# Kernel tuning notes

Measured on AMD Instinct MI355X. Metric: run time of the kernel, lower is better.

The kernel has to match this reference:

```python
import jax, jax.numpy as jnp
import numpy as np

N_CLASSES = 16
B, N = 8, 2048
F = [128, 512, 1024]
K = [6, 5, 3]
M = [512, 128, 50]
IN_DIM = 22


def get_laplacian(x):
    # exp(-squared pairwise distance) adjacency, then normalized Laplacian I - D^-1/2 A D^-1/2
    inner = jnp.matmul(x, x.transpose(0, 2, 1))            # [B,N,N]
    sq = jnp.sum(x * x, axis=-1, keepdims=True)            # [B,N,1]
    adj = jnp.exp(-(sq - 2.0 * inner + sq.transpose(0, 2, 1)))
    dinv = 1.0 / jnp.sqrt(jnp.sum(adj, axis=-1))           # [B,N]
    Lnorm = dinv[:, :, None] * adj * dinv[:, None, :]
    return jnp.eye(x.shape[1], dtype=x.dtype) - Lnorm


def cheb_conv(x, L, W, b):
    # Chebyshev recursion: x0=x, x1=Lx, x_k = 2 L x_{k-1} - x_{k-2}; out = sum_k x_k @ W_k + b
    Kk = W.shape[0]
    x0 = x
    out = jnp.einsum('bni,io->bno', x0, W[0])
    if Kk > 1:
        x1 = jnp.matmul(L, x0)
        out = out + jnp.einsum('bni,io->bno', x1, W[1])
        for k in range(2, Kk):
            x2 = 2.0 * jnp.matmul(L, x1) - x0
            out = out + jnp.einsum('bni,io->bno', x2, W[k])
            x0, x1 = x1, x2
    return out + b


def setup_inputs() -> dict:
    key = jax.random.key(0)
    ks = jax.random.split(key, 24)
    d = {}
    d['x'] = jax.random.normal(ks[0], (B, N, 6), dtype=jnp.float32)
    d['cat'] = jax.random.randint(ks[1], (B, 1), 0, N_CLASSES)
    ins = [IN_DIM, F[0], F[1]]
    for i in range(3):
        s = 1.0 / np.sqrt(ins[i] * K[i])
        d[f'cheb_w{i}'] = jax.random.normal(ks[2 + i], (K[i], ins[i], F[i]), dtype=jnp.float32) * s
        d[f'cheb_b{i}'] = jnp.zeros((F[i],), dtype=jnp.float32)
    fc_ins = [F[-1], M[0] + M[0], M[1]]
    for i in range(3):
        s = 1.0 / np.sqrt(fc_ins[i])
        d[f'fc_w{i}'] = jax.random.normal(ks[6 + i], (fc_ins[i], M[i]), dtype=jnp.float32) * s
        d[f'fc_b{i}'] = jax.random.normal(ks[10 + i], (M[i],), dtype=jnp.float32) * s
    relus = F + M
    for i in range(6):
        d[f'br{i}'] = jnp.zeros((1, N, relus[i]), dtype=jnp.float32)
    return d


def reference(x, cat, cheb_w0, cheb_b0, cheb_w1, cheb_b1, cheb_w2, cheb_b2,
              fc_w0, fc_b0, fc_w1, fc_b1, fc_w2, fc_b2,
              br0, br1, br2, br3, br4, br5):
    L = jax.lax.stop_gradient(get_laplacian(x))  # torch.no_grad in original
    cat_oh = jax.nn.one_hot(cat, N_CLASSES, dtype=x.dtype)      # [B,1,16]
    cat_oh = jnp.tile(cat_oh, (1, N, 1))                         # [B,N,16]
    out = jnp.concatenate([x, cat_oh], axis=2)                   # [B,N,22]

    cheb_ws = [cheb_w0, cheb_w1, cheb_w2]
    cheb_bs = [cheb_b0, cheb_b1, cheb_b2]
    brs = [br0, br1, br2, br3, br4, br5]
    x1 = None
    for i in range(3):
        out = cheb_conv(out, L, cheb_ws[i], cheb_bs[i])
        out = jax.nn.relu(out + brs[i])  # dropout is identity in eval
        if i == 1:
            x1 = out

    fc_ws = [fc_w0, fc_w1, fc_w2]
    fc_bs = [fc_b0, fc_b1, fc_b2]
    for i in range(3):
        if i == 1:
            out = jnp.concatenate([out, x1], axis=2)
        out = jnp.einsum('bni,io->bno', out, fc_ws[i]) + fc_bs[i]
        out = jax.nn.relu(out + brs[i + 3])
    return out
```

## Files before the change

### kernel.cpp

```cpp
#include <hip/hip_runtime.h>
#include <stdint.h>

typedef __attribute__((ext_vector_type(8))) short short8;
typedef __attribute__((ext_vector_type(4))) float f32x4;

#define DEV __device__ __forceinline__

DEV ushort f2bf(float f){ uint32_t u = __float_as_uint(f); u += 0x7fffu + ((u >> 16) & 1u); return (ushort)(u >> 16); }
DEV float bf2f(ushort h){ return __uint_as_float(((uint32_t)h) << 16); }

template<int N> DEV void wvm(){
    asm volatile("s_waitcnt vmcnt(%0)" :: "i"(N) : "memory");
}


__global__ void wt_kernel(const float* __restrict__ src, ushort* __restrict__ dst,
                          int I, int O, int Opad, int blk, int srcF){
    int idx = blockIdx.x * 256 + threadIdx.x;
    if (idx >= Opad * I) return;
    int i = idx % I, o = idx / I;
    int k = i / blk, f = i % blk;
    ushort v = 0;
    if (o < O && f < srcF) v = f2bf(src[((long)k * srcF + f) * O + o]);
    dst[idx] = v;
}

__global__ void x0t_kernel(const float* __restrict__ x, const int* __restrict__ cat,
                           ushort* __restrict__ dst){
    int idx = blockIdx.x * 256 + threadIdx.x;
    int n = idx & 2047, f = (idx >> 11) & 31, b = idx >> 16;
    ushort v = 0;
    if (f < 6) v = f2bf(x[((long)b * 2048 + n) * 6 + f]);
    else if (f < 22) v = (cat[b] == f - 6) ? (ushort)0x3f80 : (ushort)0;
    dst[idx] = v;
}

__global__ void xt_kernel(const float* __restrict__ x, float* __restrict__ xT){
    int idx = blockIdx.x * 256 + threadIdx.x;
    if (idx >= 16384) return;
    int b = idx >> 11, n = idx & 2047;
    float* dst = xT + (long)b * 6 * 2048 + n;
#pragma unroll
    for (int d = 0; d < 6; d++) dst[d * 2048] = x[(long)idx * 6 + d];
}

__global__ __launch_bounds__(256) void dinv_kernel(const float* __restrict__ xT, float* __restrict__ dinv){
    int b = blockIdx.y;
    int wave = threadIdx.x >> 6, lane = threadIdx.x & 63;
    int i0 = blockIdx.x * 16 + wave * 4;
    const float* xtb = xT + (long)b * 6 * 2048;
    float xi[4][6];
#pragma unroll
    for (int ii = 0; ii < 4; ii++)
#pragma unroll
        for (int d = 0; d < 6; d++) xi[ii][d] = xtb[d * 2048 + i0 + ii];
    float s[4] = {0.f, 0.f, 0.f, 0.f};
#pragma unroll 2
    for (int jj = 0; jj < 32; jj++){
        int j = jj * 64 + lane;
        float xd[6];
#pragma unroll
        for (int d = 0; d < 6; d++) xd[d] = xtb[d * 2048 + j];
#pragma unroll
        for (int ii = 0; ii < 4; ii++){
            float a = 0.0f;
#pragma unroll
            for (int d = 0; d < 6; d++){ float t = xi[ii][d] - xd[d]; a += t * t; }
            s[ii] += __expf(-a);
        }
    }
#pragma unroll
    for (int ii = 0; ii < 4; ii++){
#pragma unroll
        for (int o = 32; o > 0; o >>= 1) s[ii] += __shfl_xor(s[ii], o);
    }
    if (lane == 0){
#pragma unroll
        for (int ii = 0; ii < 4; ii++) dinv[(b << 11) + i0 + ii] = rsqrtf(s[ii]);
    }
}

__global__ __launch_bounds__(256) void lap_kernel(const float* __restrict__ x, const float* __restrict__ dinv,
                                                  ushort* __restrict__ L){
    int b = blockIdx.z;
    int i0 = blockIdx.y * 32 + (threadIdx.x >> 6) * 8;
    int j0 = blockIdx.x * 512 + (threadIdx.x & 63) * 8;
    const float* xb = x + (long)b * 2048 * 6;
    const float* dv = dinv + (b << 11);
    f32x4 v[12];
    const f32x4* src = (const f32x4*)(xb + (long)j0 * 6);
#pragma unroll
    for (int c = 0; c < 12; c++) v[c] = src[c];
    const float* xj = (const float*)v;
    f32x4 dj0 = *(const f32x4*)(dv + j0);
    f32x4 dj1 = *(const f32x4*)(dv + j0 + 4);
    float dj[8] = {dj0[0], dj0[1], dj0[2], dj0[3], dj1[0], dj1[1], dj1[2], dj1[3]};
    ushort* out = L + ((long)b << 22) + (long)i0 * 2048 + j0;
#pragma unroll
    for (int ii = 0; ii < 8; ii++){
        const int i = i0 + ii;
        float xi[6];
#pragma unroll
        for (int d = 0; d < 6; d++) xi[d] = xb[i * 6 + d];
        const float di = dv[i];
        short8 o;
#pragma unroll
        for (int jj = 0; jj < 8; jj++){
            float a = 0.0f;
#pragma unroll
            for (int d = 0; d < 6; d++){ float t = xi[d] - xj[jj * 6 + d]; a += t * t; }
            float val = -di * dj[jj] * __expf(-a);
            if (i == j0 + jj) val += 1.0f;
            o[jj] = (short)f2bf(val);
        }
        *(short8*)(out + (long)ii * 2048) = o;
    }
}

__global__ void ts_kernel(const ushort* __restrict__ src, ushort* __restrict__ dst,
                          int F, int KF){
    int b = blockIdx.z;
    int i0 = blockIdx.y * 32;
    int k = i0 / F, f0 = i0 % F;
    int n0 = blockIdx.x * 64;
    __shared__ ushort t[32][66];
    const ushort* s = src + (((long)k * 8 + b) * F + f0) * 2048 + n0;
    int r = threadIdx.x >> 3, c8 = (threadIdx.x & 7) * 8;
    *(short8*)&t[r][c8] = *(const short8*)(s + (long)r * 2048 + c8);
    __syncthreads();
    int c = threadIdx.x >> 2, r8 = (threadIdx.x & 3) * 8;
    short8 v;
#pragma unroll
    for (int j = 0; j < 8; j++) v[j] = (short)t[r8 + j][c];
    *(short8*)(dst + ((long)b * 2048 + n0 + c) * KF + i0 + r8) = v;
}

__global__ void copy_x1_kernel(const ushort* __restrict__ src, ushort* __restrict__ dst){
    int idx = blockIdx.x * 256 + threadIdx.x;
    int r = idx >> 6, c = (idx & 63) * 8;
    *(short8*)(dst + (long)r * 1024 + 512 + c) = *(const short8*)(src + (long)r * 1536 + c);
}

template<int BM, int BN, int WR, int WC, int MODE>
__global__ __launch_bounds__(256) void gemm2(
    const ushort* __restrict__ A, int lda, long sA,
    const ushort* __restrict__ BT, int ldb, long sB,
    ushort* __restrict__ C, int ldc, long sC,
    int K,
    const ushort* __restrict__ Xp, long sX,
    const float* __restrict__ bias, const float* __restrict__ br, int brF,
    float* __restrict__ outF)
{
    constexpr int WM = BM / WR, WN = BN / WC, FM = WM / 16, FN = WN / 16;
    constexpr int ACH = BM / 16;
    constexpr int NCH = (BM + BN) / 16;
    __shared__ __align__(16) ushort As[BM * 32];
    __shared__ __align__(16) ushort Bs[BN * 32];
    const int tid = threadIdx.x, lane = tid & 63, wave = tid >> 6;
    const int wr = wave / WC, wc = wave % WC;
    const int bm0 = blockIdx.x * BM, bn0 = blockIdx.y * BN;
    const long z = blockIdx.z;
    A += z * sA; BT += z * sB;
    if (MODE != 4) C += z * sC;
    if (MODE == 1) Xp += z * sX;

    f32x4 acc[FM][FN];
#pragma unroll
    for (int m = 0; m < FM; m++)
#pragma unroll
        for (int n = 0; n < FN; n++) acc[m][n] = f32x4{0.f, 0.f, 0.f, 0.f};

    const int crow = lane >> 2;
    const int ccol = (lane & 3) * 8;

    for (int kt = 0; kt < K; kt += 32){
#pragma unroll
        for (int c = wave; c < NCH; c += 4){
            const ushort* gsrc;
            ushort* ldst;
            if (c < ACH){
                ldst = &As[c * 512];
                gsrc = A + (long)(bm0 + c * 16 + crow) * lda + kt + ccol;
            } else {
                ldst = &Bs[(c - ACH) * 512];
                gsrc = BT + (long)(bn0 + (c - ACH) * 16 + crow) * ldb + kt + ccol;
            }
            __builtin_amdgcn_global_load_lds(
                (const __attribute__((address_space(1))) void*)gsrc,
                (__attribute__((address_space(3))) void*)ldst, 16, 0, 0);
        }
        __syncthreads();
        const int kg = (lane >> 4) * 8;
        short8 af[FM], bfr[FN];
#pragma unroll
        for (int m = 0; m < FM; m++)
            af[m] = *(const short8*)&As[(wr * WM + m * 16 + (lane & 15)) * 32 + kg];
#pragma unroll
        for (int n = 0; n < FN; n++)
            bfr[n] = *(const short8*)&Bs[(wc * WN + n * 16 + (lane & 15)) * 32 + kg];
#pragma unroll
        for (int m = 0; m < FM; m++)
#pragma unroll
            for (int n = 0; n < FN; n++)
                acc[m][n] = __builtin_amdgcn_mfma_f32_16x16x32_bf16(af[m], bfr[n], acc[m][n], 0, 0, 0);
        __syncthreads();
    }

#pragma unroll
    for (int m = 0; m < FM; m++){
        const int r0 = bm0 + wr * WM + m * 16 + ((lane >> 4) << 2);
#pragma unroll
        for (int n = 0; n < FN; n++){
            const int col = bn0 + wc * WN + n * 16 + (lane & 15);
#pragma unroll
            for (int j = 0; j < 4; j++){
                const int r = r0 + j;
                float v = acc[m][n][j];
                if (MODE == 0){
                    C[(long)r * ldc + col] = f2bf(v);
                } else if (MODE == 1){
                    float p = bf2f(Xp[(long)r * ldc + col]);
                    C[(long)r * ldc + col] = f2bf(2.0f * v - p);
                } else if (MODE == 2){
                    float o = v + bias[r] + br[(long)col * brF + r];
                    C[(long)r * ldc + col] = f2bf(fmaxf(o, 0.0f));
                } else if (MODE == 3){
                    float o = v + bias[col] + br[(long)(r & 2047) * brF + col];
                    C[(long)r * ldc + col] = f2bf(fmaxf(o, 0.0f));
                } else {
                    if (col < 50){
                        float o = v + bias[col] + br[(long)(r & 2047) * 50 + col];
                        outF[(long)r * 50 + col] = fmaxf(o, 0.0f);
                    }
                }
            }
        }
    }
}

template<int BM, int BN, int MODE>
__global__ __launch_bounds__(256) void gmv(
    const ushort* __restrict__ A, int lda, long sA,
    const ushort* __restrict__ BT, int ldb, long sB,
    ushort* __restrict__ C, int ldc, long sC,
    int K,
    const ushort* __restrict__ Xp, long sX)
{
    constexpr int WM = BM / 2, WN = BN / 2, FM = WM / 16, FN = WN / 16;
    constexpr int ACH = BM / 8;
    constexpr int NCH = (BM + BN) / 8;
    constexpr int LPW = NCH / 4;
    static_assert(NCH % 4 == 0, "uniform loads per wave");
    __shared__ __align__(16) ushort lds[3 * (BM + BN) * 64];
    const int tid = threadIdx.x, lane = tid & 63, wave = tid >> 6;
    const int wr = wave >> 1, wc = wave & 1;
    const long z = blockIdx.x;
    const int bm0 = blockIdx.y * BM, bn0 = blockIdx.z * BN;
    A += z * sA; BT += z * sB; C += z * sC;
    if (MODE == 1) Xp += z * sX;
    const int NT = K >> 6;

    const int srow = lane >> 3;
    const int kloc = ((lane & 7) ^ srow) * 8;

    auto stage = [&](int u, int sel){
        ushort* dst0 = lds + sel * (BM + BN) * 64;
#pragma unroll
        for (int i = 0; i < LPW; i++){
            int c = i * 4 + wave;
            ushort* ldst = dst0 + c * 512;
            const ushort* src;
            if (c < ACH) src = A + (long)(bm0 + c * 8 + srow) * lda + u * 64 + kloc;
            else         src = BT + (long)(bn0 + (c - ACH) * 8 + srow) * ldb + u * 64 + kloc;
            __builtin_amdgcn_global_load_lds(
                (const __attribute__((address_space(1))) void*)src,
                (__attribute__((address_space(3))) void*)ldst, 16, 0, 0);
        }
    };

    f32x4 acc[FM][FN];
#pragma unroll
    for (int m = 0; m < FM; m++)
#pragma unroll
        for (int n = 0; n < FN; n++) acc[m][n] = f32x4{0.f, 0.f, 0.f, 0.f};

    stage(0, 0);
    if (NT > 1) stage(1, 1);

    int sel = 0;
    for (int u = 0; u < NT; u++){
        if (u + 1 < NT) wvm<LPW>(); else wvm<0>();
        __builtin_amdgcn_sched_barrier(0);
        __builtin_amdgcn_s_barrier();
        __builtin_amdgcn_sched_barrier(0);
        const char* base = (const char*)lds + sel * (BM + BN) * 128;
        const int hi = (lane >> 4) << 4;
        short8 af[FM], bfr[FN];
#pragma unroll
        for (int h = 0; h < 2; h++){
            const int kb = h * 64 + hi;
#pragma unroll
            for (int m = 0; m < FM; m++){
                int row = wr * WM + m * 16 + (lane & 15);
                af[m] = *(const short8*)(base + row * 128 + (kb ^ ((row & 7) << 4)));
            }
#pragma unroll
            for (int n = 0; n < FN; n++){
                int row = BM + wc * WN + n * 16 + (lane & 15);
                bfr[n] = *(const short8*)(base + row * 128 + (kb ^ ((row & 7) << 4)));
            }
            __builtin_amdgcn_s_setprio(1);
#pragma unroll
            for (int m = 0; m < FM; m++)
#pragma unroll
                for (int n = 0; n < FN; n++)
                    acc[m][n] = __builtin_amdgcn_mfma_f32_16x16x32_bf16(af[m], bfr[n], acc[m][n], 0, 0, 0);
            __builtin_amdgcn_s_setprio(0);
        }
        if (u + 2 < NT) stage(u + 2, (u + 2) % 3);
        sel = (sel == 2) ? 0 : sel + 1;
    }

#pragma unroll
    for (int m = 0; m < FM; m++){
        const int r0 = bm0 + wr * WM + m * 16 + ((lane >> 4) << 2);
#pragma unroll
        for (int n = 0; n < FN; n++){
            const int col = bn0 + wc * WN + n * 16 + (lane & 15);
#pragma unroll
            for (int j = 0; j < 4; j++){
                const int r = r0 + j;
                float v = acc[m][n][j];
                if (MODE == 0){
                    C[(long)r * ldc + col] = f2bf(v);
                } else {
                    float p = bf2f(Xp[(long)r * ldc + col]);
                    C[(long)r * ldc + col] = f2bf(2.0f * v - p);
                }
            }
        }
    }
}

template<int MODE, int SWZ>
__global__ __launch_bounds__(256) void gd(
    const ushort* __restrict__ A, int lda, long sA,
    const ushort* __restrict__ BT, int ldb, long sB,
    ushort* __restrict__ C, int ldc, long sC,
    int K,
    const ushort* __restrict__ Xp, long sX,
    const float* __restrict__ bias, const float* __restrict__ br, int brF)
{
    __shared__ __align__(16) ushort lds[2 * 256 * 64];
    const int tid = threadIdx.x, lane = tid & 63, wave = tid >> 6;
    const int wr = wave >> 1, wc = wave & 1;
    const int bm0 = (SWZ ? blockIdx.y : blockIdx.x) * 128;
    const int bn0 = (SWZ ? blockIdx.z : blockIdx.y) * 128;
    const long z = SWZ ? blockIdx.x : blockIdx.z;
    A += z * sA; BT += z * sB; C += z * sC;
    if (MODE == 1) Xp += z * sX;
    const int NT = K >> 6;

    const int srow = lane >> 3;
    const int kloc = ((lane & 7) ^ srow) * 8;

    auto stage = [&](int u, int sel){
        ushort* dst0 = lds + sel * 16384;
#pragma unroll
        for (int i = 0; i < 8; i++){
            int c = i * 4 + wave;
            const ushort* src = (c < 16)
                ? A + (long)(bm0 + c * 8 + srow) * lda + (long)u * 64 + kloc
                : BT + (long)(bn0 + (c - 16) * 8 + srow) * ldb + (long)u * 64 + kloc;
            __builtin_amdgcn_global_load_lds(
                (const __attribute__((address_space(1))) void*)src,
                (__attribute__((address_space(3))) void*)(dst0 + c * 512), 16, 0, 0);
        }
    };

    f32x4 acc[4][4];
#pragma unroll
    for (int m = 0; m < 4; m++)
#pragma unroll
        for (int n = 0; n < 4; n++) acc[m][n] = f32x4{0.f, 0.f, 0.f, 0.f};

    stage(0, 0);
    if (NT > 1) stage(1, 1);
    wvm<8>();
    __builtin_amdgcn_sched_barrier(0);
    __builtin_amdgcn_s_barrier();
    __builtin_amdgcn_sched_barrier(0);

    for (int u = 0; u < NT; u++){
        const char* Ab = (const char*)lds + (u & 1) * 32768;
        const char* Bb = Ab + 16384;
        const int hi = (lane >> 4) << 4;
        short8 af[4], bf[4];
#pragma unroll
        for (int m = 0; m < 4; m++){
            int row = wr * 64 + m * 16 + (lane & 15);
            af[m] = *(const short8*)(Ab + row * 128 + (hi ^ ((row & 7) << 4)));
        }
#pragma unroll
        for (int n = 0; n < 4; n++){
            int row = wc * 64 + n * 16 + (lane & 15);
            bf[n] = *(const short8*)(Bb + row * 128 + (hi ^ ((row & 7) << 4)));
        }
        if (u >= 1 && u + 1 < NT) stage(u + 1, (u + 1) & 1);
        __builtin_amdgcn_s_setprio(1);
#pragma unroll
        for (int m = 0; m < 4; m++)
#pragma unroll
            for (int n = 0; n < 4; n++)
                acc[m][n] = __builtin_amdgcn_mfma_f32_16x16x32_bf16(af[m], bf[n], acc[m][n], 0, 0, 0);
        __builtin_amdgcn_s_setprio(0);
#pragma unroll
        for (int m = 0; m < 4; m++){
            int row = wr * 64 + m * 16 + (lane & 15);
            af[m] = *(const short8*)(Ab + row * 128 + ((64 + hi) ^ ((row & 7) << 4)));
        }
#pragma unroll
        for (int n = 0; n < 4; n++){
            int row = wc * 64 + n * 16 + (lane & 15);
            bf[n] = *(const short8*)(Bb + row * 128 + ((64 + hi) ^ ((row & 7) << 4)));
        }
        __builtin_amdgcn_s_setprio(1);
#pragma unroll
        for (int m = 0; m < 4; m++)
#pragma unroll
            for (int n = 0; n < 4; n++)
                acc[m][n] = __builtin_amdgcn_mfma_f32_16x16x32_bf16(af[m], bf[n], acc[m][n], 0, 0, 0);
        __builtin_amdgcn_s_setprio(0);
        wvm<0>();
        __builtin_amdgcn_sched_barrier(0);
        __builtin_amdgcn_s_barrier();
        __builtin_amdgcn_sched_barrier(0);
    }

#pragma unroll
    for (int m = 0; m < 4; m++){
        const int r0 = bm0 + wr * 64 + m * 16 + ((lane >> 4) << 2);
#pragma unroll
        for (int n = 0; n < 4; n++){
            const int col = bn0 + wc * 64 + n * 16 + (lane & 15);
#pragma unroll
            for (int j = 0; j < 4; j++){
                const int r = r0 + j;
                float v = acc[m][n][j];
                if (MODE == 0){
                    C[(long)r * ldc + col] = f2bf(v);
                } else if (MODE == 1){
                    float p = bf2f(Xp[(long)r * ldc + col]);
                    C[(long)r * ldc + col] = f2bf(2.0f * v - p);
                } else if (MODE == 2){
                    float o = v + bias[r] + br[(long)col * brF + r];
                    C[(long)r * ldc + col] = f2bf(fmaxf(o, 0.0f));
                } else {
                    float o = v + bias[col] + br[(long)(r & 2047) * brF + col];
                    C[(long)r * ldc + col] = f2bf(fmaxf(o, 0.0f));
                }
            }
        }
    }
}


extern "C" void kernel_launch(void* const* d_in, const int* in_sizes, int n_in,
                              void* d_out, int out_size, void* d_ws, size_t ws_size,
                              hipStream_t stream){
    const float* x   = (const float*)d_in[0];
    const int*   cat = (const int*)d_in[1];
    const float* cw0 = (const float*)d_in[2];
    const float* cb0 = (const float*)d_in[3];
    const float* cw1 = (const float*)d_in[4];
    const float* cb1 = (const float*)d_in[5];
    const float* cw2 = (const float*)d_in[6];
    const float* cb2 = (const float*)d_in[7];
    const float* fw0 = (const float*)d_in[8];
    const float* fb0 = (const float*)d_in[9];
    const float* fw1 = (const float*)d_in[10];
    const float* fb1 = (const float*)d_in[11];
    const float* fw2 = (const float*)d_in[12];
    const float* fb2 = (const float*)d_in[13];
    const float* br0 = (const float*)d_in[14];
    const float* br1 = (const float*)d_in[15];
    const float* br2 = (const float*)d_in[16];
    const float* br3 = (const float*)d_in[17];
    const float* br4 = (const float*)d_in[18];
    const float* br5 = (const float*)d_in[19];
    float* out = (float*)d_out;
    (void)in_sizes; (void)n_in; (void)out_size; (void)ws_size;

    char* ws = (char*)d_ws;
    long off = 0;
    auto take = [&](long bytes){ char* p = ws + off; off += (bytes + 255) & ~255L; return p; };
    ushort* Lb   = (ushort*)take(8L * 2048 * 2048 * 2);
    float*  din  = (float*) take(8L * 2048 * 4);
    float*  XT   = (float*) take(8L * 6 * 2048 * 4);
    ushort* W0T  = (ushort*)take(128L * 192 * 2);
    ushort* W1T  = (ushort*)take(512L * 640 * 2);
    ushort* W2T  = (ushort*)take(1024L * 1536 * 2);
    ushort* WF0T = (ushort*)take(512L * 1024 * 2);
    ushort* WF1T = (ushort*)take(128L * 1024 * 2);
    ushort* WF2T = (ushort*)take(64L * 128 * 2);
    ushort* ST0T = (ushort*)take(6L * 8 * 32 * 2048 * 2);
    ushort* S0   = (ushort*)take(16384L * 192 * 2);
    ushort* ST1T = (ushort*)take(5L * 8 * 128 * 2048 * 2);
    ushort* S1   = (ushort*)take(16384L * 640 * 2);
    ushort* ST2T = (ushort*)take(3L * 8 * 512 * 2048 * 2);
    ushort* S2   = (ushort*)take(16384L * 1536 * 2);
    ushort* X3 = Lb;
    ushort* CC = ST2T;
    ushort* H5 = ST0T;

    const long NN = 2048L * 2048;
    const long s0k = 8L * 32 * 2048,  s0b = 32L * 2048;
    const long s1k = 8L * 128 * 2048, s1b = 128L * 2048;
    const long s2k = 8L * 512 * 2048, s2b = 512L * 2048;

    wt_kernel<<<(128 * 192 + 255) / 256, 256, 0, stream>>>(cw0, W0T, 192, 128, 128, 32, 22);
    wt_kernel<<<(512 * 640 + 255) / 256, 256, 0, stream>>>(cw1, W1T, 640, 512, 512, 128, 128);
    wt_kernel<<<(1024 * 1536 + 255) / 256, 256, 0, stream>>>(cw2, W2T, 1536, 1024, 1024, 512, 512);
    wt_kernel<<<(512 * 1024 + 255) / 256, 256, 0, stream>>>(fw0, WF0T, 1024, 512, 512, 1024, 1024);
    wt_kernel<<<(128 * 1024 + 255) / 256, 256, 0, stream>>>(fw1, WF1T, 1024, 128, 128, 1024, 1024);
    wt_kernel<<<(64 * 128 + 255) / 256, 256, 0, stream>>>(fw2, WF2T, 128, 50, 64, 128, 128);

    x0t_kernel<<<2048, 256, 0, stream>>>(x, cat, ST0T);
    xt_kernel<<<64, 256, 0, stream>>>(x, XT);
    dinv_kernel<<<dim3(128, 8), 256, 0, stream>>>(XT, din);
    lap_kernel<<<dim3(4, 64, 8), 256, 0, stream>>>(x, din, Lb);

    gmv<32, 32, 0><<<dim3(8, 1, 64), 256, 0, stream>>>(
        ST0T, 2048, s0b, Lb, 2048, NN, ST0T + s0k, 2048, s0b, 2048, nullptr, 0);
    for (int k = 2; k < 6; k++)
        gmv<32, 32, 1><<<dim3(8, 1, 64), 256, 0, stream>>>(
            ST0T + (k - 1) * s0k, 2048, s0b, Lb, 2048, NN, ST0T + k * s0k, 2048, s0b, 2048,
            ST0T + (k - 2) * s0k, s0b);
    ts_kernel<<<dim3(32, 6, 8), 256, 0, stream>>>(ST0T, S0, 32, 192);
    gemm2<64, 128, 2, 2, 2><<<dim3(2, 16, 8), 256, 0, stream>>>(
        W0T, 192, 0, S0, 192, 2048L * 192, ST1T, 2048, s1b, 192, nullptr, 0, cb0, br0, 128, nullptr);

    gmv<128, 32, 0><<<dim3(8, 1, 64), 256, 0, stream>>>(
        ST1T, 2048, s1b, Lb, 2048, NN, ST1T + s1k, 2048, s1b, 2048, nullptr, 0);
    for (int k = 2; k < 5; k++)
        gmv<128, 32, 1><<<dim3(8, 1, 64), 256, 0, stream>>>(
            ST1T + (k - 1) * s1k, 2048, s1b, Lb, 2048, NN, ST1T + k * s1k, 2048, s1b, 2048,
            ST1T + (k - 2) * s1k, s1b);
    ts_kernel<<<dim3(32, 20, 8), 256, 0, stream>>>(ST1T, S1, 128, 640);
    gd<2, 1><<<dim3(8, 4, 16), 256, 0, stream>>>(
        W1T, 640, 0, S1, 640, 2048L * 640, ST2T, 2048, s2b, 640, nullptr, 0, cb1, br1, 512);

    gd<0, 1><<<dim3(8, 4, 16), 256, 0, stream>>>(
        ST2T, 2048, s2b, Lb, 2048, NN, ST2T + s2k, 2048, s2b, 2048, nullptr, 0, nullptr, nullptr, 0);
    gd<1, 1><<<dim3(8, 4, 16), 256, 0, stream>>>(
        ST2T + s2k, 2048, s2b, Lb, 2048, NN, ST2T + 2 * s2k, 2048, s2b, 2048,
        ST2T, s2b, nullptr, nullptr, 0);
    ts_kernel<<<dim3(32, 48, 8), 256, 0, stream>>>(ST2T, S2, 512, 1536);
    gd<3, 0><<<dim3(128, 8, 1), 256, 0, stream>>>(
        S2, 1536, 0, W2T, 1536, 0, X3, 1024, 0, 1536, nullptr, 0, cb2, br2, 1024);

    gd<3, 0><<<dim3(128, 4, 1), 256, 0, stream>>>(
        X3, 1024, 0, WF0T, 1024, 0, CC, 1024, 0, 1024, nullptr, 0, fb0, br3, 512);
    copy_x1_kernel<<<4096, 256, 0, stream>>>(S2, CC);
    gemm2<128, 64, 2, 2, 3><<<dim3(128, 2, 1), 256, 0, stream>>>(
        CC, 1024, 0, WF1T, 1024, 0, H5, 128, 0, 1024, nullptr, 0, fb1, br4, 128, nullptr);
    gemm2<128, 64, 2, 2, 4><<<dim3(128, 1, 1), 256, 0, stream>>>(
        H5, 128, 0, WF2T, 128, 0, nullptr, 0, 0, 128, nullptr, 0, fb2, br5, 50, out);
}
```

Measured before the change: 443.9 us.

## Add 256x256-tile double-buffered GEMM for the layer-3 weight projection

Adds a new g256 kernel with 512 threads, 256x256 output tiles, direct global-to-LDS loads into an XOR-swizzled, double-buffered LDS layout, and MFMA 16x16x32 bf16 with setprio around the math. It replaces the gd<3,0> launch for the 16384x1024x1536 projection. The goal is more operand reuse per byte loaded and fewer blocks. The cost is 128KB of LDS per block, heavy register use and only 256 blocks. The degree-reduction shuffle order is also reordered slightly.

```diff
diff --git a/kernel.cpp b/kernel.cpp
--- a/kernel.cpp
+++ b/kernel.cpp
@@ -72,7 +72,8 @@
 #pragma unroll
     for (int ii = 0; ii < 4; ii++){
 #pragma unroll
-        for (int o = 32; o > 0; o >>= 1) s[ii] += __shfl_xor(s[ii], o);
+        for (int o = 16; o > 0; o >>= 1) s[ii] += __shfl_xor(s[ii], o);
+        s[ii] += __shfl_xor(s[ii], 32);
     }
     if (lane == 0){
 #pragma unroll
@@ -459,6 +460,93 @@
                     float o = v + bias[col] + br[(long)(r & 2047) * brF + col];
                     C[(long)r * ldc + col] = f2bf(fmaxf(o, 0.0f));
                 }
+            }
+        }
+    }
+}
+
+__global__ __launch_bounds__(512, 2) void g256(
+    const ushort* __restrict__ A, int lda,
+    const ushort* __restrict__ BT, int ldb,
+    ushort* __restrict__ C, int ldc,
+    int K,
+    const float* __restrict__ bias, const float* __restrict__ br, int brF)
+{
+    __shared__ __align__(16) ushort lds[65536];
+    const int lane = threadIdx.x & 63, wave = threadIdx.x >> 6;
+    const int wr = wave >> 2, wc = wave & 3;
+    const int bm0 = blockIdx.x * 256, bn0 = blockIdx.y * 256;
+    const int NT = K >> 6;
+
+    const int srow = lane >> 3;
+    const int kloc = ((lane & 7) ^ srow) * 8;
+
+    auto stage = [&](int u, int sel){
+        ushort* dst0 = lds + sel * 32768;
+#pragma unroll
+        for (int i = 0; i < 8; i++){
+            int c = i * 8 + wave;
+            const ushort* src = (c < 32)
+                ? A + (long)(bm0 + c * 8 + srow) * lda + (long)u * 64 + kloc
+                : BT + (long)(bn0 + (c - 32) * 8 + srow) * ldb + (long)u * 64 + kloc;
+            __builtin_amdgcn_global_load_lds(
+                (const __attribute__((address_space(1))) void*)src,
+                (__attribute__((address_space(3))) void*)(dst0 + c * 512), 16, 0, 0);
+        }
+    };
+
+    f32x4 acc[8][4];
+#pragma unroll
+    for (int m = 0; m < 8; m++)
+#pragma unroll
+        for (int n = 0; n < 4; n++) acc[m][n] = f32x4{0.f, 0.f, 0.f, 0.f};
+
+    stage(0, 0);
+    if (NT > 1) stage(1, 1);
+
+    for (int u = 0; u < NT; u++){
+        if (u == 0 && NT > 1) wvm<8>(); else wvm<0>();
+        __builtin_amdgcn_sched_barrier(0);
+        __builtin_amdgcn_s_barrier();
+        __builtin_amdgcn_sched_barrier(0);
+        if (u >= 1 && u + 1 < NT) stage(u + 1, (u + 1) & 1);
+        const char* base = (const char*)lds + (u & 1) * 65536;
+        const int hi = (lane >> 4) << 4;
+        short8 af[8], bf[4];
+#pragma unroll
+        for (int h = 0; h < 2; h++){
+            const int kb = h * 64 + hi;
+#pragma unroll
+            for (int m = 0; m < 8; m++){
+                int row = wr * 128 + m * 16 + (lane & 15);
+                af[m] = *(const short8*)(base + row * 128 + (kb ^ ((row & 7) << 4)));
+            }
+#pragma unroll
+            for (int n = 0; n < 4; n++){
+                int row = 256 + wc * 64 + n * 16 + (lane & 15);
+                bf[n] = *(const short8*)(base + row * 128 + (kb ^ ((row & 7) << 4)));
+            }
+            __builtin_amdgcn_s_setprio(1);
+#pragma unroll
+            for (int m = 0; m < 8; m++)
+#pragma unroll
+                for (int n = 0; n < 4; n++)
+                    acc[m][n] = __builtin_amdgcn_mfma_f32_16x16x32_bf16(af[m], bf[n], acc[m][n], 0, 0, 0);
+            __builtin_amdgcn_s_setprio(0);
+        }
+    }
+
+#pragma unroll
+    for (int m = 0; m < 8; m++){
+        const int r0 = bm0 + wr * 128 + m * 16 + ((lane >> 4) << 2);
+#pragma unroll
+        for (int n = 0; n < 4; n++){
+            const int col = bn0 + wc * 64 + n * 16 + (lane & 15);
+#pragma unroll
+            for (int j = 0; j < 4; j++){
+                const int r = r0 + j;
+                float o = acc[m][n][j] + bias[col] + br[(long)(r & 2047) * brF + col];
+                C[(long)r * ldc + col] = f2bf(fmaxf(o, 0.0f));
             }
         }
     }
@@ -556,8 +644,8 @@
         ST2T + s2k, 2048, s2b, Lb, 2048, NN, ST2T + 2 * s2k, 2048, s2b, 2048,
         ST2T, s2b, nullptr, nullptr, 0);
     ts_kernel<<<dim3(32, 48, 8), 256, 0, stream>>>(ST2T, S2, 512, 1536);
-    gd<3, 0><<<dim3(128, 8, 1), 256, 0, stream>>>(
-        S2, 1536, 0, W2T, 1536, 0, X3, 1024, 0, 1536, nullptr, 0, cb2, br2, 1024);
+    g256<<<dim3(64, 4), 512, 0, stream>>>(
+        S2, 1536, W2T, 1536, X3, 1024, 1536, cb2, br2, 1024);
 
     gd<3, 0><<<dim3(128, 4, 1), 256, 0, stream>>>(
         X3, 1024, 0, WF0T, 1024, 0, CC, 1024, 0, 1024, nullptr, 0, fb0, br3, 512);
```

Result: slower. 463.6 us (+4.4%).
